# Optimization experiments

Measured on AMD Instinct MI355X. Metric: run time of the kernel, lower is better.

The kernel has to match this reference:

```python
import jax, jax.numpy as jnp
import numpy as np
import math
from jax import lax


def _conv(x, w, b, stride=1, pad=0, groups=1):
    # x: [B,C,H,W], w: [O, C//groups, kh, kw] (OIHW)
    out = lax.conv_general_dilated(x, w, (stride, stride), [(pad, pad), (pad, pad)],
                                   feature_group_count=groups,
                                   dimension_numbers=('NCHW', 'OIHW', 'NCHW'))
    return out + b.reshape(1, -1, 1, 1)


def _shared_conv(x, k2d, b, stride=1, pad=0):
    # SharedConv: one [k,k] kernel shared across all channels (depthwise), scalar bias
    C = x.shape[1]
    w = jnp.broadcast_to(k2d[None, None], (C, 1) + k2d.shape)
    out = lax.conv_general_dilated(x, w, (stride, stride), [(pad, pad), (pad, pad)],
                                   feature_group_count=C,
                                   dimension_numbers=('NCHW', 'OIHW', 'NCHW'))
    return out + b


def _bn(x, g, b, m, v, eps=1e-5):
    scale = (g / jnp.sqrt(v + eps)).reshape(1, -1, 1, 1)
    return (x - m.reshape(1, -1, 1, 1)) * scale + b.reshape(1, -1, 1, 1)


def _leaky(x, s=0.01):
    return jnp.where(x >= 0, x, s * x)


def _max_leaky(x, t, s):
    # cap values above threshold with leaky slope
    return jnp.where(x <= t, x, t + s * (x - t))


def _min_leaky(x, t, s):
    # cap values below threshold with leaky slope
    return jnp.where(x >= t, x, t + s * (x - t))


def _mode_pool(x, k=11, padding=1):
    # histogram mode pooling: 17 bins over quantized values, stride 1
    xp = jnp.pad(x, ((0, 0), (0, 0), (padding, padding), (padding, padding)))
    bins = jnp.clip(jnp.round(xp * 16.0), 0.0, 16.0).astype(jnp.int32)
    oh = jax.nn.one_hot(bins, 17, dtype=x.dtype)           # [B,C,Hp,Wp,17]
    counts = lax.reduce_window(oh, 0.0, lax.add, (1, 1, k, k, 1), (1, 1, 1, 1, 1), 'VALID')
    return jnp.argmax(counts, axis=-1).astype(x.dtype) / 16.0


def _emphase(x, w, k=11):
    # EmphaseLocal: unsharp-style local emphasis with per-channel learnable scale
    s = lax.reduce_window(x, 0.0, lax.add, (1, 1, k, k), (1, 1, 1, 1), 'SAME')
    avg = s / float(k * k)
    return x + w.reshape(1, -1, 1, 1) * (x - avg)


def setup_inputs() -> dict:
    key = jax.random.key(0)
    ks = jax.random.split(key, 20)
    f32 = jnp.float32
    B, Cin, H, W = 2, 3, 512, 512
    C2 = 64  # half_out_channels * 2
    return {
        'x': jax.random.uniform(ks[0], (B, Cin, H, W), f32),
        'w1': jax.random.normal(ks[1], (C2, Cin, 1, 1), f32) * 0.1,
        'b1': jax.random.normal(ks[2], (C2,), f32) * 0.05,
        'w2': jax.random.normal(ks[3], (C2, 2, 1, 1), f32) * 0.1,  # groups=32
        'b2': jax.random.normal(ks[4], (C2,), f32) * 0.05,
        'down_k': jax.random.normal(ks[5], (3, 3), f32) * 0.1,
        'down_b': jax.random.normal(ks[6], (), f32) * 0.05,
        'ft_gamma': 1.0 + jax.random.normal(ks[7], (C2,), f32) * 0.1,
        'ft_beta': jax.random.normal(ks[8], (C2,), f32) * 0.05,
        'ft_mean': jax.random.normal(ks[9], (C2,), f32) * 0.05,
        'ft_var': jax.random.uniform(ks[10], (C2,), f32, 0.5, 1.5),
        'ft_k': jax.random.normal(ks[11], (1, 1), f32) * 0.5 + 1.0,
        'ft_b': jax.random.normal(ks[12], (), f32) * 0.05,
        'emph_w': jax.random.normal(ks[13], (C2,), f32) * 0.1,
        'interp_k': jax.random.normal(ks[14], (5, 5), f32) * 0.1,
        'interp_b': jax.random.normal(ks[15], (), f32) * 0.05,
        'i_gamma': 1.0 + jax.random.normal(ks[16], (C2,), f32) * 0.1,
        'i_beta': jax.random.normal(ks[17], (C2,), f32) * 0.05,
        'i_mean': jax.random.normal(ks[18], (C2,), f32) * 0.05,
        'i_var': jax.random.uniform(ks[19], (C2,), f32, 0.5, 1.5),
    }


def reference(x, w1, b1, w2, b2, down_k, down_b,
              ft_gamma, ft_beta, ft_mean, ft_var, ft_k, ft_b, emph_w,
              interp_k, interp_b, i_gamma, i_beta, i_mean, i_var):
    B, _, H, W = x.shape
    C2 = w1.shape[0]
    # prepare: ColorDownsample(16) -> ModePool2d(11,1,1) -> 1x1 conv -> MaxLeakyReLU -> grouped 1x1 conv -> MinLeakyReLU
    xd = jnp.round(x * 255.0 / 16.0) * 16.0 / 256.0
    h = _mode_pool(xd, k=11, padding=1)                 # [B,Cin,H-8,W-8]
    h = _max_leaky(_conv(h, w1, b1), 0.1, 0.01)
    groups = C2 // w2.shape[1]
    d = _min_leaky(_conv(h, w2, b2, groups=groups), 0.1, 0.01)
    score = jnp.zeros((B, C2, H, W), x.dtype)
    n = math.floor(math.log(min(d.shape[2], d.shape[3]), 3))
    for _ in range(n):
        # downgrade: shared 3x3 stride-3 conv + leaky
        d = _leaky(_shared_conv(d, down_k, down_b, stride=3, pad=1))
        # zoom back to full resolution, then interpolate branch (shared 5x5 conv + BN + leaky)
        z = jax.image.resize(d, (B, C2, H, W), method='bilinear')
        z = _bn(_shared_conv(z, interp_k, interp_b, pad=2), i_gamma, i_beta, i_mean, i_var)
        score = score + _leaky(z)
    # ft applied 3 times with shared weights: BN -> shared 1x1 conv -> EmphaseLocal
    for _ in range(3):
        s = _bn(score, ft_gamma, ft_beta, ft_mean, ft_var)
        s = _shared_conv(s, ft_k, ft_b)
        score = _emphase(s, emph_w, k=11)
    return score
```

## Files before the change

kernel.cpp:

```cpp
#include <hip/hip_runtime.h>

#define NB 2
#define CIN 3
#define HH 512
#define WW 512
#define C2 64
#define HM 504

typedef float v2f  __attribute__((ext_vector_type(2)));
typedef float v2fu __attribute__((ext_vector_type(2), aligned(4)));

__global__ __launch_bounds__(256) void k_mode(const float* __restrict__ x,
                                              unsigned char* __restrict__ hmode) {
  __shared__ unsigned char tile[26 * 26];
  int bc  = blockIdx.z;
  int ty0 = blockIdx.y * 16, tx0 = blockIdx.x * 16;
  const float* src = x + (size_t)bc * HH * WW;
  for (int i = threadIdx.x; i < 26 * 26; i += 256) {
    int r = i / 26, cl = i % 26;
    int Y = ty0 + r, X = tx0 + cl;
    unsigned char v = 0;
    if (Y >= 1 && Y <= HH && X >= 1 && X <= WW) {
      float val = src[(Y - 1) * WW + (X - 1)];
      float q = rintf((val * 255.0f) / 16.0f);
      q = fminf(fmaxf(q, 0.0f), 16.0f);
      v = (unsigned char)(int)q;
    }
    tile[i] = v;
  }
  __syncthreads();
  int ty = threadIdx.x >> 4, tx = threadIdx.x & 15;
  int oy = ty0 + ty, ox = tx0 + tx;
  if (oy >= HM || ox >= HM) return;
  unsigned long long w0 = 0, w1 = 0, w2 = 0;
  for (int dy = 0; dy < 11; dy++) {
    #pragma unroll
    for (int dx = 0; dx < 11; dx++) {
      int b = tile[(ty + dy) * 26 + tx + dx];
      unsigned long long inc = 1ull << ((b & 7) * 8);
      if (b < 8) w0 += inc;
      else if (b < 16) w1 += inc;
      else w2 += inc;
    }
  }
  int best = -1, bestb = 0;
  #pragma unroll
  for (int b = 0; b < 17; b++) {
    int cnt;
    if (b < 8)       cnt = (int)((w0 >> (b * 8)) & 0xff);
    else if (b < 16) cnt = (int)((w1 >> ((b - 8) * 8)) & 0xff);
    else             cnt = (int)(w2 & 0xff);
    if (cnt > best) { best = cnt; bestb = b; }
  }
  hmode[bc * HM * HM + oy * HM + ox] = (unsigned char)bestb;
}

__global__ __launch_bounds__(256) void k_prepare(const unsigned char* __restrict__ hmode,
                                                 const float* __restrict__ w1,
                                                 const float* __restrict__ b1,
                                                 const float* __restrict__ w2,
                                                 const float* __restrict__ b2,
                                                 const float* __restrict__ down_k,
                                                 const float* __restrict__ down_b,
                                                 float* __restrict__ d1) {
  int bc = blockIdx.y;
  int b  = bc >> 6;
  int c  = bc & 63;
  int pix = blockIdx.x * 256 + threadIdx.x;
  if (pix >= 168 * 168) return;
  int oy = pix / 168, ox = pix % 168;
  int c0 = (c >> 1) << 1;
  float w1a0 = w1[c0 * 3], w1a1 = w1[c0 * 3 + 1], w1a2 = w1[c0 * 3 + 2], b1a = b1[c0];
  float w1b0 = w1[(c0 + 1) * 3], w1b1 = w1[(c0 + 1) * 3 + 1], w1b2 = w1[(c0 + 1) * 3 + 2], b1b = b1[c0 + 1];
  float w2a = w2[c * 2], w2b = w2[c * 2 + 1], b2c = b2[c];
  float kb = *down_b;
  const unsigned char* h0p = hmode + (b * 3 + 0) * HM * HM;
  const unsigned char* h1p = hmode + (b * 3 + 1) * HM * HM;
  const unsigned char* h2p = hmode + (b * 3 + 2) * HM * HM;
  float acc = 0.0f;
  #pragma unroll
  for (int ky = 0; ky < 3; ky++) {
    int y = 3 * oy - 1 + ky;
    if (y < 0 || y >= HM) continue;
    #pragma unroll
    for (int kx = 0; kx < 3; kx++) {
      int xx = 3 * ox - 1 + kx;
      if (xx < 0 || xx >= HM) continue;
      int o = y * HM + xx;
      float hh0 = h0p[o] * (1.0f / 16.0f);
      float hh1 = h1p[o] * (1.0f / 16.0f);
      float hh2 = h2p[o] * (1.0f / 16.0f);
      float a0 = w1a0 * hh0 + w1a1 * hh1 + w1a2 * hh2 + b1a;
      float a1 = w1b0 * hh0 + w1b1 * hh1 + w1b2 * hh2 + b1b;
      a0 = (a0 <= 0.1f) ? a0 : 0.1f + 0.01f * (a0 - 0.1f);
      a1 = (a1 <= 0.1f) ? a1 : 0.1f + 0.01f * (a1 - 0.1f);
      float v = w2a * a0 + w2b * a1 + b2c;
      v = (v >= 0.1f) ? v : 0.1f + 0.01f * (v - 0.1f);
      acc += down_k[ky * 3 + kx] * v;
    }
  }
  float r = acc + kb;
  r = (r >= 0.0f) ? r : 0.01f * r;
  d1[bc * 168 * 168 + pix] = r;
}

__global__ __launch_bounds__(256) void k_down(const float* __restrict__ din,
                                              float* __restrict__ dout,
                                              const float* __restrict__ down_k,
                                              const float* __restrict__ down_b,
                                              int S, int So) {
  int bc = blockIdx.y;
  int pix = blockIdx.x * 256 + threadIdx.x;
  if (pix >= So * So) return;
  int oy = pix / So, ox = pix % So;
  const float* p = din + bc * S * S;
  float acc = 0.0f;
  #pragma unroll
  for (int ky = 0; ky < 3; ky++) {
    int y = 3 * oy - 1 + ky;
    if (y < 0 || y >= S) continue;
    #pragma unroll
    for (int kx = 0; kx < 3; kx++) {
      int xx = 3 * ox - 1 + kx;
      if (xx < 0 || xx >= S) continue;
      acc += down_k[ky * 3 + kx] * p[y * S + xx];
    }
  }
  float r = acc + *down_b;
  r = (r >= 0.0f) ? r : 0.01f * r;
  dout[bc * So * So + pix] = r;
}

__global__ __launch_bounds__(256) void k_lut(float2* __restrict__ lutpk) {
  int idx = blockIdx.x * 256 + threadIdx.x;
  if (idx >= 5 * 512) return;
  int lvl = idx >> 9, Y = idx & 511;
  const int Ls[5] = {168, 56, 19, 7, 3};
  int L = Ls[lvl];
  float f = (Y + 0.5f) * ((float)L / 512.0f) - 0.5f;
  f = fminf(fmaxf(f, 0.0f), (float)(L - 1));
  int y0 = (int)f;
  float w = f - (float)y0;
  lutpk[idx] = make_float2(__int_as_float(y0), w);
}

__global__ __launch_bounds__(256, 4) void k_score(const float* __restrict__ d1,
                                                  const float* __restrict__ d2,
                                                  const float* __restrict__ d3,
                                                  const float* __restrict__ d4,
                                                  const float* __restrict__ d5,
                                                  const float2* __restrict__ lutpk,
                                                  const float* __restrict__ interp_k,
                                                  const float* __restrict__ interp_b,
                                                  const float* __restrict__ i_gamma,
                                                  const float* __restrict__ i_beta,
                                                  const float* __restrict__ i_mean,
                                                  const float* __restrict__ i_var,
                                                  float* __restrict__ score) {
  __shared__ float xrow[24 * 132];
  __shared__ float kap[64 * 36];
  __shared__ int   abase[64];

  int bc = blockIdx.y;
  int c  = bc & 63;
  int tile = blockIdx.x;
  int tyi = tile >> 2, txi = tile & 3;
  int ty0 = tyi * 64, tx0 = txi * 128;
  float K[25];
  #pragma unroll
  for (int i = 0; i < 25; i++)
    K[i] = __int_as_float(__builtin_amdgcn_readfirstlane(__float_as_int(interp_k[i])));
  float ib  = __int_as_float(__builtin_amdgcn_readfirstlane(__float_as_int(*interp_b)));
  float isc = i_gamma[c] * rsqrtf(i_var[c] + 1e-5f);
  float ibe = i_beta[c] - i_mean[c] * isc;
  int tid = threadIdx.x;
  int oyl = (tid >> 4) << 2, oxl = (tid & 15) << 3;
  float acc[4][8];
  #pragma unroll
  for (int i = 0; i < 4; i++)
    #pragma unroll
    for (int j = 0; j < 8; j++) acc[i][j] = 0.0f;

  const float* dls[5] = {d1, d2, d3, d4, d5};
  const int Ls[5]  = {168, 56, 19, 7, 3};
  const int RLs[5] = {24, 10, 5, 3, 3};

  auto fillLevel = [&](int l) {
    int L = Ls[l], RR = RLs[l];
    const float* dp = dls[l] + bc * L * L;
    const float2* lp = lutpk + (l << 9);
    int Ylo = max(ty0 - 2, 0);
    int r0 = __float_as_int(lp[Ylo].x);
    {
      int y = tid >> 2, rr = tid & 3;
      int Y = ty0 + y;
      float kv0 = 0.0f, kv1 = 0.0f, kv2 = 0.0f, kv3 = 0.0f, kv4 = 0.0f;
      int ab = -1;
      #pragma unroll
      for (int ky = 0; ky < 5; ky++) {
        int yy = Y + ky - 2;
        if (yy >= 0 && yy < 512) {
          float2 pk = lp[yy];
          int a0 = __float_as_int(pk.x);
          float wv = pk.y;
          if (ab < 0) ab = a0;
          float cf = 0.0f;
          if (a0 - ab == rr)     cf += 1.0f - wv;
          if (a0 + 1 - ab == rr) cf += wv;
          kv0 += cf * K[ky * 5 + 0];
          kv1 += cf * K[ky * 5 + 1];
          kv2 += cf * K[ky * 5 + 2];
          kv3 += cf * K[ky * 5 + 3];
          kv4 += cf * K[ky * 5 + 4];
        }
      }
      float* kp = &kap[y * 36 + rr * 8];
      kp[0] = kv0; kp[1] = kv1; kp[2] = kv2; kp[3] = kv3; kp[4] = kv4;
      if (rr == 0) abase[y] = ab - r0;
    }
    for (int i = tid; i < RR * 132; i += 256) {
      int r = i / 132, xx = i - r * 132;
      int X = tx0 - 2 + xx;
      float v = 0.0f;
      if (X >= 0 && X < 512) {
        float2 pk = lp[X];
        int ix = __float_as_int(pk.x);
        float wx = pk.y;
        int gr = min(r0 + r, L - 1);
        const float* rp = dp + gr * L + ix;
        float v0 = rp[0], v1 = rp[1];
        v = v0 + wx * (v1 - v0);
      }
      xrow[r * 132 + xx] = v;
    }
  };

  auto convAcc = [&](int rspan, int rlim) {
    #pragma unroll
    for (int i = 0; i < 4; i++) {
      int y = oyl + i;
      int ab = abase[y];
      float t[8];
      #pragma unroll
      for (int j = 0; j < 8; j++) t[j] = 0.0f;
      for (int rr = 0; rr < rspan; rr++) {
        int row = min(ab + rr, rlim);
        const float* xp = &xrow[row * 132 + oxl];
        float4 A = *(const float4*)xp;
        float4 B = *(const float4*)(xp + 4);
        float4 Cx = *(const float4*)(xp + 8);
        const float* kp = &kap[y * 36 + rr * 8];
        float4 kk = *(const float4*)kp;
        float k4v = kp[4];
        float wnd[12] = {A.x, A.y, A.z, A.w, B.x, B.y, B.z, B.w, Cx.x, Cx.y, Cx.z, Cx.w};
        #pragma unroll
        for (int j = 0; j < 8; j++)
          t[j] += kk.x * wnd[j] + kk.y * wnd[j + 1] + kk.z * wnd[j + 2] +
                  kk.w * wnd[j + 3] + k4v * wnd[j + 4];
      }
      #pragma unroll
      for (int j = 0; j < 8; j++) {
        float v = (t[j] + ib) * isc + ibe;
        v = (v >= 0.0f) ? v : 0.01f * v;
        acc[i][j] += v;
      }
    }
  };

  #pragma unroll 1
  for (int l = 0; l < 5; l++) {
    if (l) __syncthreads();
    fillLevel(l);
    __syncthreads();
    if (l == 0) convAcc(4, RLs[0] - 1);
    else        convAcc(3, RLs[l] - 1);
  }

  float* op = score + bc * 512 * 512;
  #pragma unroll
  for (int i = 0; i < 4; i++) {
    int Y = ty0 + oyl + i;
    float* orow = op + Y * 512 + tx0 + oxl;
    *(float4*)(orow)     = make_float4(acc[i][0], acc[i][1], acc[i][2], acc[i][3]);
    *(float4*)(orow + 4) = make_float4(acc[i][4], acc[i][5], acc[i][6], acc[i][7]);
  }
}

__global__ __launch_bounds__(256, 3) void k_ft_pipe(const float* __restrict__ s_in,
                                                    float* __restrict__ s_out,
                                                    const float* __restrict__ ft_gamma,
                                                    const float* __restrict__ ft_beta,
                                                    const float* __restrict__ ft_mean,
                                                    const float* __restrict__ ft_var,
                                                    const float* __restrict__ ft_k,
                                                    const float* __restrict__ ft_b,
                                                    const float* __restrict__ emph_w) {
  __shared__ float brow1[2][524];
  __shared__ float brow2[2][524];
  __shared__ float brow3[2][524];

  const int bc = blockIdx.y;
  const int c  = bc & 63;
  const int R0 = blockIdx.x << 7;
  const int mstart = R0 - 15;

  const float sc  = ft_gamma[c] * rsqrtf(ft_var[c] + 1e-5f);
  const float fk = *ft_k, fb = *ft_b;
  const float Aff = sc * fk;
  const float Cc  = (ft_beta[c] - ft_mean[c] * sc) * fk + fb;
  const float w   = emph_w[c];
  const float opw = 1.0f + w;
  const float okw = w * (1.0f / 121.0f);

  const int tid = threadIdx.x;
  const int x0  = tid << 1;

  const float* sp = s_in + ((size_t)bc << 18) + x0;
  float*       op = s_out + ((size_t)bc << 18) + x0;

  if (tid < 72) {
    int a = tid / 24, pb = (tid / 12) & 1, e = tid % 12;
    int idx = (e < 6) ? e : (512 + e);
    float* base = (a == 0) ? &brow1[pb][0] : (a == 1) ? &brow2[pb][0] : &brow3[pb][0];
    base[idx] = 0.0f;
  }

  auto ldraw = [&](int row) -> v2f {
    int rc = min(max(row, 0), 511);
    return *(const v2f*)(sp + ((size_t)rc << 9));
  };

  auto rowsum = [&](const float* b) -> v2f {
    const float* p = b + x0;
    v2f w0 = *(const v2f*)(p);
    v2f w1 = *(const v2f*)(p + 2);
    v2f w2 = *(const v2f*)(p + 4);
    v2f w3 = *(const v2f*)(p + 6);
    v2f w4 = *(const v2f*)(p + 8);
    v2f w5 = *(const v2f*)(p + 10);
    v2f w6 = *(const v2f*)(p + 12);
    float smid = ((w1.x + w1.y) + (w2.x + w2.y)) +
                 ((w3.x + w3.y) + (w4.x + w4.y)) + (w5.x + w5.y);
    v2f r;
    r.x = smid + w0.y;
    r.y = smid + w6.x;
    return r;
  };

  v2f cs1 = (v2f)0.0f, cs2 = (v2f)0.0f, cs3 = (v2f)0.0f;
  v2f out1p = (v2f)0.0f, out2p = (v2f)0.0f;

  v2f r2[12], r3[12];
  #pragma unroll
  for (int k = 0; k < 12; k++) { r2[k] = (v2f)0.0f; r3[k] = (v2f)0.0f; }

  v2f gf  = ldraw(mstart);
  v2f gfa = ldraw(mstart + 1);
  v2f go  = ldraw(mstart - 11);
  v2f gc  = ldraw(mstart - 5);

  #pragma unroll 1
  for (int ii = 0; ii < 14; ++ii) {
    #pragma unroll
    for (int j = 0; j < 12; ++j) {
      const int i = ii * 12 + j;
      const int m = mstart + i;
      v2f gf_n2 = ldraw(m + 2);
      v2f go_n  = ldraw(m - 10);
      v2f gc_n  = ldraw(m - 4);

      const int p = j & 1;

      {
        v2f u1f = (m >= 0 && m < 512) ? (gf * Aff + Cc) : (v2f)0.0f;
        int r = m - 11;
        v2f u1o = (r >= mstart && r >= 0 && r < 512) ? (go * Aff + Cc) : (v2f)0.0f;
        cs1 += u1f - u1o;
        *(v2f*)(&brow1[p][6 + x0]) = cs1;
      }
      {
        v2f u2s = out1p * Aff + Cc;
        v2f u2or = r2[(j + 1) % 12];
        r2[j] = u2s;
        int rf = m - 6;
        v2f u2f = (rf >= 0 && rf < 512) ? u2s : (v2f)0.0f;
        int r = m - 17;
        v2f u2o = (r >= mstart - 6 && r >= 0 && r < 512) ? u2or : (v2f)0.0f;
        cs2 += u2f - u2o;
        *(v2f*)(&brow2[p][6 + x0]) = cs2;
      }
      {
        v2f u3s = out2p * Aff + Cc;
        v2f u3or = r3[(j + 1) % 12];
        r3[j] = u3s;
        int rf = m - 12;
        v2f u3f = (rf >= 0 && rf < 512) ? u3s : (v2f)0.0f;
        int r = m - 23;
        v2f u3o = (r >= mstart - 12 && r >= 0 && r < 512) ? u3or : (v2f)0.0f;
        cs3 += u3f - u3o;
        *(v2f*)(&brow3[p][6 + x0]) = cs3;
      }
      __syncthreads();
      {
        int rc1 = m - 5;
        v2f u1c = (rc1 >= 0 && rc1 < 512) ? (gc * Aff + Cc) : (v2f)0.0f;
        v2f B1 = rowsum(&brow1[p][0]);
        out1p = u1c * opw - B1 * okw;
      }
      {
        int rc2 = m - 11;
        v2f u2cr = r2[(j + 7) % 12];
        v2f u2c = (rc2 >= mstart - 6 && rc2 >= 0 && rc2 < 512) ? u2cr : (v2f)0.0f;
        v2f B2 = rowsum(&brow2[p][0]);
        out2p = u2c * opw - B2 * okw;
      }
      {
        int rc3 = m - 17;
        v2f u3cr = r3[(j + 7) % 12];
        v2f u3c = (rc3 >= mstart - 12 && rc3 >= 0 && rc3 < 512) ? u3cr : (v2f)0.0f;
        v2f B3 = rowsum(&brow3[p][0]);
        v2f o3 = u3c * opw - B3 * okw;
        if (i >= 32 && i < 160)
          *(v2f*)(op + ((size_t)(m - 17) << 9)) = o3;
      }
      gf = gfa; gfa = gf_n2; go = go_n; gc = gc_n;
    }
  }
}

extern "C" void kernel_launch(void* const* d_in, const int* in_sizes, int n_in,
                              void* d_out, int out_size, void* d_ws, size_t ws_size,
                              hipStream_t stream) {
  const float* x        = (const float*)d_in[0];
  const float* w1       = (const float*)d_in[1];
  const float* b1       = (const float*)d_in[2];
  const float* w2       = (const float*)d_in[3];
  const float* b2       = (const float*)d_in[4];
  const float* down_k   = (const float*)d_in[5];
  const float* down_b   = (const float*)d_in[6];
  const float* ft_gamma = (const float*)d_in[7];
  const float* ft_beta  = (const float*)d_in[8];
  const float* ft_mean  = (const float*)d_in[9];
  const float* ft_var   = (const float*)d_in[10];
  const float* ft_k     = (const float*)d_in[11];
  const float* ft_b     = (const float*)d_in[12];
  const float* emph_w   = (const float*)d_in[13];
  const float* interp_k = (const float*)d_in[14];
  const float* interp_b = (const float*)d_in[15];
  const float* i_gamma  = (const float*)d_in[16];
  const float* i_beta   = (const float*)d_in[17];
  const float* i_mean   = (const float*)d_in[18];
  const float* i_var    = (const float*)d_in[19];
  float* out = (float*)d_out;

  char* ws = (char*)d_ws;
  size_t off = 0;
  auto alloc = [&](size_t bytes) { size_t r = off; off += (bytes + 255) & ~(size_t)255; return r; };
  unsigned char* hmode = (unsigned char*)(ws + alloc((size_t)NB * CIN * HM * HM));
  float* d1 = (float*)(ws + alloc((size_t)NB * C2 * 168 * 168 * 4));
  float* d2 = (float*)(ws + alloc((size_t)NB * C2 * 56 * 56 * 4));
  float* d3 = (float*)(ws + alloc((size_t)NB * C2 * 19 * 19 * 4));
  float* d4 = (float*)(ws + alloc((size_t)NB * C2 * 7 * 7 * 4));
  float* d5 = (float*)(ws + alloc((size_t)NB * C2 * 3 * 3 * 4));
  float* s0 = (float*)(ws + alloc((size_t)NB * C2 * 512 * 512 * 4));
  float2* lutpk = (float2*)(ws + alloc((size_t)5 * 512 * 8));

  k_mode<<<dim3(32, 32, NB * CIN), 256, 0, stream>>>(x, hmode);
  k_lut<<<10, 256, 0, stream>>>(lutpk);
  k_prepare<<<dim3((168 * 168 + 255) / 256, NB * C2), 256, 0, stream>>>(
      hmode, w1, b1, w2, b2, down_k, down_b, d1);
  k_down<<<dim3((56 * 56 + 255) / 256, NB * C2), 256, 0, stream>>>(d1, d2, down_k, down_b, 168, 56);
  k_down<<<dim3((19 * 19 + 255) / 256, NB * C2), 256, 0, stream>>>(d2, d3, down_k, down_b, 56, 19);
  k_down<<<dim3((7 * 7 + 255) / 256, NB * C2), 256, 0, stream>>>(d3, d4, down_k, down_b, 19, 7);
  k_down<<<dim3((3 * 3 + 255) / 256, NB * C2), 256, 0, stream>>>(d4, d5, down_k, down_b, 7, 3);
  k_score<<<dim3(32, NB * C2), 256, 0, stream>>>(d1, d2, d3, d4, d5, lutpk,
                                                 interp_k, interp_b,
                                                 i_gamma, i_beta, i_mean, i_var, s0);
  k_ft_pipe<<<dim3(4, NB * C2), 256, 0, stream>>>(s0, out, ft_gamma, ft_beta, ft_mean,
                                                  ft_var, ft_k, ft_b, emph_w);
}
```

Measured before the change: 544.3 us.

## Process two rows per barrier in ft pipeline and pad score LDS rows

The fused ft pipeline kernel now advances two image rows per iteration. Each stage's column-sum buffer is double-buffered per row pair, so only one __syncthreads is needed for every two rows, which halves barrier count along the pipeline and reshuffles the stage delays. Separately, the k_score shared-memory input rows get a padded stride and a skewed index of 4 extra floats every 32 columns, meant to reduce LDS bank conflicts on the float4 window loads. The cost is more LDS, register pressure from the doubled live state, and delicate index bookkeeping.

```diff
diff --git a/kernel.cpp b/kernel.cpp
--- a/kernel.cpp
+++ b/kernel.cpp
@@ -144,6 +144,8 @@
   lutpk[idx] = make_float2(__int_as_float(y0), w);
 }
 
+#define XI(cc) ((cc) + ((((cc) >> 5)) << 2))
+#define XSTR 148
 __global__ __launch_bounds__(256, 4) void k_score(const float* __restrict__ d1,
                                                   const float* __restrict__ d2,
                                                   const float* __restrict__ d3,
@@ -157,7 +159,7 @@
                                                   const float* __restrict__ i_mean,
                                                   const float* __restrict__ i_var,
                                                   float* __restrict__ score) {
-  __shared__ float xrow[24 * 132];
+  __shared__ float xrow[24 * XSTR];
   __shared__ float kap[64 * 36];
   __shared__ int   abase[64];
 
@@ -175,6 +177,8 @@
   float ibe = i_beta[c] - i_mean[c] * isc;
   int tid = threadIdx.x;
   int oyl = (tid >> 4) << 2, oxl = (tid & 15) << 3;
+  const int pA = XI(oxl);
+  const int pC = XI(oxl + 8);
   float acc[4][8];
   #pragma unroll
   for (int i = 0; i < 4; i++)
@@ -231,7 +235,7 @@
         float v0 = rp[0], v1 = rp[1];
         v = v0 + wx * (v1 - v0);
       }
-      xrow[r * 132 + xx] = v;
+      xrow[r * XSTR + XI(xx)] = v;
     }
   };
 
@@ -245,10 +249,10 @@
       for (int j = 0; j < 8; j++) t[j] = 0.0f;
       for (int rr = 0; rr < rspan; rr++) {
         int row = min(ab + rr, rlim);
-        const float* xp = &xrow[row * 132 + oxl];
-        float4 A = *(const float4*)xp;
-        float4 B = *(const float4*)(xp + 4);
-        float4 Cx = *(const float4*)(xp + 8);
+        const float* xp = &xrow[row * XSTR];
+        float4 A = *(const float4*)(xp + pA);
+        float4 B = *(const float4*)(xp + pA + 4);
+        float4 Cx = *(const float4*)(xp + pC);
         const float* kp = &kap[y * 36 + rr * 8];
         float4 kk = *(const float4*)kp;
         float k4v = kp[4];
@@ -295,9 +299,9 @@
                                                     const float* __restrict__ ft_k,
                                                     const float* __restrict__ ft_b,
                                                     const float* __restrict__ emph_w) {
-  __shared__ float brow1[2][524];
-  __shared__ float brow2[2][524];
-  __shared__ float brow3[2][524];
+  __shared__ float brow1[2][2][524];
+  __shared__ float brow2[2][2][524];
+  __shared__ float brow3[2][2][524];
 
   const int bc = blockIdx.y;
   const int c  = bc & 63;
@@ -318,10 +322,11 @@
   const float* sp = s_in + ((size_t)bc << 18) + x0;
   float*       op = s_out + ((size_t)bc << 18) + x0;
 
-  if (tid < 72) {
-    int a = tid / 24, pb = (tid / 12) & 1, e = tid % 12;
+  if (tid < 144) {
+    int a = tid / 48, rem = tid % 48;
+    int pb = rem / 24, rw = (rem / 12) & 1, e = rem % 12;
     int idx = (e < 6) ? e : (512 + e);
-    float* base = (a == 0) ? &brow1[pb][0] : (a == 1) ? &brow2[pb][0] : &brow3[pb][0];
+    float* base = (a == 0) ? &brow1[pb][rw][0] : (a == 1) ? &brow2[pb][rw][0] : &brow3[pb][rw][0];
     base[idx] = 0.0f;
   }
 
@@ -348,82 +353,106 @@
   };
 
   v2f cs1 = (v2f)0.0f, cs2 = (v2f)0.0f, cs3 = (v2f)0.0f;
-  v2f out1p = (v2f)0.0f, out2p = (v2f)0.0f;
+  v2f o1a = (v2f)0.0f, o1b = (v2f)0.0f;
+  v2f o2a = (v2f)0.0f, o2b = (v2f)0.0f;
 
   v2f r2[12], r3[12];
   #pragma unroll
   for (int k = 0; k < 12; k++) { r2[k] = (v2f)0.0f; r3[k] = (v2f)0.0f; }
 
-  v2f gf  = ldraw(mstart);
-  v2f gfa = ldraw(mstart + 1);
-  v2f go  = ldraw(mstart - 11);
-  v2f gc  = ldraw(mstart - 5);
+  v2f gf0 = ldraw(mstart),      gf1 = ldraw(mstart + 1);
+  v2f go0 = ldraw(mstart - 11), go1 = ldraw(mstart - 10);
+  v2f gc0 = ldraw(mstart - 5),  gc1 = ldraw(mstart - 4);
 
   #pragma unroll 1
   for (int ii = 0; ii < 14; ++ii) {
     #pragma unroll
-    for (int j = 0; j < 12; ++j) {
-      const int i = ii * 12 + j;
-      const int m = mstart + i;
-      v2f gf_n2 = ldraw(m + 2);
-      v2f go_n  = ldraw(m - 10);
-      v2f gc_n  = ldraw(m - 4);
+    for (int j = 0; j < 6; ++j) {
+      const int i = ii * 6 + j;
+      const int m = mstart + 2 * i;
+      v2f nf0 = ldraw(m + 2), nf1 = ldraw(m + 3);
+      v2f no0 = ldraw(m - 9), no1 = ldraw(m - 8);
+      v2f nc0 = ldraw(m - 3), nc1 = ldraw(m - 2);
 
       const int p = j & 1;
 
       {
-        v2f u1f = (m >= 0 && m < 512) ? (gf * Aff + Cc) : (v2f)0.0f;
-        int r = m - 11;
-        v2f u1o = (r >= mstart && r >= 0 && r < 512) ? (go * Aff + Cc) : (v2f)0.0f;
-        cs1 += u1f - u1o;
-        *(v2f*)(&brow1[p][6 + x0]) = cs1;
+        v2f u1fa = (m >= 0 && m < 512) ? (gf0 * Aff + Cc) : (v2f)0.0f;
+        int ra = m - 11;
+        v2f u1oa = (ra >= mstart && ra >= 0 && ra < 512) ? (go0 * Aff + Cc) : (v2f)0.0f;
+        cs1 += u1fa - u1oa;
+        *(v2f*)(&brow1[p][0][6 + x0]) = cs1;
+        v2f u1fb = (m + 1 >= 0 && m + 1 < 512) ? (gf1 * Aff + Cc) : (v2f)0.0f;
+        int rb = m - 10;
+        v2f u1ob = (rb >= mstart && rb >= 0 && rb < 512) ? (go1 * Aff + Cc) : (v2f)0.0f;
+        cs1 += u1fb - u1ob;
+        *(v2f*)(&brow1[p][1][6 + x0]) = cs1;
       }
       {
-        v2f u2s = out1p * Aff + Cc;
-        v2f u2or = r2[(j + 1) % 12];
-        r2[j] = u2s;
-        int rf = m - 6;
-        v2f u2f = (rf >= 0 && rf < 512) ? u2s : (v2f)0.0f;
-        int r = m - 17;
-        v2f u2o = (r >= mstart - 6 && r >= 0 && r < 512) ? u2or : (v2f)0.0f;
-        cs2 += u2f - u2o;
-        *(v2f*)(&brow2[p][6 + x0]) = cs2;
+        v2f u2a = o1a * Aff + Cc;
+        v2f u2b = o1b * Aff + Cc;
+        v2f olda = r2[(2 * j + 1) % 12];
+        v2f oldb = r2[(2 * j + 2) % 12];
+        r2[2 * j] = u2a; r2[(2 * j + 1) % 12] = u2b;
+        int rfa = m - 7, rsa = m - 18;
+        v2f aadd = (rfa >= 0 && rfa < 512) ? u2a : (v2f)0.0f;
+        v2f asub = (rsa >= mstart - 7 && rsa >= 0 && rsa < 512) ? olda : (v2f)0.0f;
+        cs2 += aadd - asub;
+        *(v2f*)(&brow2[p][0][6 + x0]) = cs2;
+        int rfb = m - 6, rsb = m - 17;
+        v2f badd = (rfb >= 0 && rfb < 512) ? u2b : (v2f)0.0f;
+        v2f bsub = (rsb >= mstart - 7 && rsb >= 0 && rsb < 512) ? oldb : (v2f)0.0f;
+        cs2 += badd - bsub;
+        *(v2f*)(&brow2[p][1][6 + x0]) = cs2;
       }
       {
-        v2f u3s = out2p * Aff + Cc;
-        v2f u3or = r3[(j + 1) % 12];
-        r3[j] = u3s;
-        int rf = m - 12;
-        v2f u3f = (rf >= 0 && rf < 512) ? u3s : (v2f)0.0f;
-        int r = m - 23;
-        v2f u3o = (r >= mstart - 12 && r >= 0 && r < 512) ? u3or : (v2f)0.0f;
-        cs3 += u3f - u3o;
-        *(v2f*)(&brow3[p][6 + x0]) = cs3;
+        v2f u3a = o2a * Aff + Cc;
+        v2f u3b = o2b * Aff + Cc;
+        v2f olda = r3[(2 * j + 1) % 12];
+        v2f oldb = r3[(2 * j + 2) % 12];
+        r3[2 * j] = u3a; r3[(2 * j + 1) % 12] = u3b;
+        int rfa = m - 14, rsa = m - 25;
+        v2f aadd = (rfa >= 0 && rfa < 512) ? u3a : (v2f)0.0f;
+        v2f asub = (rsa >= mstart - 14 && rsa >= 0 && rsa < 512) ? olda : (v2f)0.0f;
+        cs3 += aadd - asub;
+        *(v2f*)(&brow3[p][0][6 + x0]) = cs3;
+        int rfb = m - 13, rsb = m - 24;
+        v2f badd = (rfb >= 0 && rfb < 512) ? u3b : (v2f)0.0f;
+        v2f bsub = (rsb >= mstart - 14 && rsb >= 0 && rsb < 512) ? oldb : (v2f)0.0f;
+        cs3 += badd - bsub;
+        *(v2f*)(&brow3[p][1][6 + x0]) = cs3;
       }
       __syncthreads();
       {
-        int rc1 = m - 5;
-        v2f u1c = (rc1 >= 0 && rc1 < 512) ? (gc * Aff + Cc) : (v2f)0.0f;
-        v2f B1 = rowsum(&brow1[p][0]);
-        out1p = u1c * opw - B1 * okw;
+        int ra = m - 5, rb = m - 4;
+        v2f u1ca = (ra >= 0 && ra < 512) ? (gc0 * Aff + Cc) : (v2f)0.0f;
+        v2f u1cb = (rb >= 0 && rb < 512) ? (gc1 * Aff + Cc) : (v2f)0.0f;
+        o1a = u1ca * opw - rowsum(&brow1[p][0][0]) * okw;
+        o1b = u1cb * opw - rowsum(&brow1[p][1][0]) * okw;
       }
       {
-        int rc2 = m - 11;
-        v2f u2cr = r2[(j + 7) % 12];
-        v2f u2c = (rc2 >= mstart - 6 && rc2 >= 0 && rc2 < 512) ? u2cr : (v2f)0.0f;
-        v2f B2 = rowsum(&brow2[p][0]);
-        out2p = u2c * opw - B2 * okw;
+        int ra = m - 12, rb = m - 11;
+        v2f ua = r2[(2 * j + 7) % 12];
+        v2f ub = r2[(2 * j + 8) % 12];
+        v2f u2ca = (ra >= mstart - 7 && ra >= 0 && ra < 512) ? ua : (v2f)0.0f;
+        v2f u2cb = (rb >= mstart - 7 && rb >= 0 && rb < 512) ? ub : (v2f)0.0f;
+        o2a = u2ca * opw - rowsum(&brow2[p][0][0]) * okw;
+        o2b = u2cb * opw - rowsum(&brow2[p][1][0]) * okw;
       }
       {
-        int rc3 = m - 17;
-        v2f u3cr = r3[(j + 7) % 12];
-        v2f u3c = (rc3 >= mstart - 12 && rc3 >= 0 && rc3 < 512) ? u3cr : (v2f)0.0f;
-        v2f B3 = rowsum(&brow3[p][0]);
-        v2f o3 = u3c * opw - B3 * okw;
-        if (i >= 32 && i < 160)
-          *(v2f*)(op + ((size_t)(m - 17) << 9)) = o3;
-      }
-      gf = gfa; gfa = gf_n2; go = go_n; gc = gc_n;
+        int ra = m - 19, rb = m - 18;
+        v2f ua = r3[(2 * j + 7) % 12];
+        v2f ub = r3[(2 * j + 8) % 12];
+        v2f u3ca = (ra >= mstart - 14 && ra >= 0 && ra < 512) ? ua : (v2f)0.0f;
+        v2f u3cb = (rb >= mstart - 14 && rb >= 0 && rb < 512) ? ub : (v2f)0.0f;
+        v2f oa = u3ca * opw - rowsum(&brow3[p][0][0]) * okw;
+        v2f ob = u3cb * opw - rowsum(&brow3[p][1][0]) * okw;
+        if (i >= 17 && i <= 80) {
+          *(v2f*)(op + ((size_t)(m - 19) << 9)) = oa;
+          *(v2f*)(op + ((size_t)(m - 18) << 9)) = ob;
+        }
+      }
+      gf0 = nf0; gf1 = nf1; go0 = no0; go1 = no1; gc0 = nc0; gc1 = nc1;
     }
   }
 }
```

Measured after the change: 545.7 us. Within noise of the previous version (+0.3%).
